# Performance work log

Measured on AMD Instinct MI355X. Metric: run time of the kernel, lower is better.

Reference implementation:

```python
import jax, jax.numpy as jnp
import numpy as np

HEADS = 24
KV_HEADS = 6
HEAD_DIM = 64


def _partial_rope(x, cos, sin):
    # x: [B, H, S, head_dim]; cos/sin: [S, rot_dim]; rotate first rot_dim dims
    rot_dim = cos.shape[-1]
    x_rot, x_pass = x[..., :rot_dim], x[..., rot_dim:]
    half = rot_dim // 2
    # use_real_unbind_dim=-2: reshape (..., 2, half) then unbind -> first/second half
    x_real, x_imag = x_rot[..., :half], x_rot[..., half:]
    x_rotated = jnp.concatenate([-x_imag, x_real], axis=-1)
    out = x_rot * cos[None, None] + x_rotated * sin[None, None]
    return jnp.concatenate([out, x_pass], axis=-1)


def setup_inputs() -> dict:
    key = jax.random.key(0)
    ks = jax.random.split(key, 8)
    B, S, D = 2, 2048, 1536
    kv_dim = KV_HEADS * HEAD_DIM
    rot_dim = 32
    hidden_states = jax.random.normal(ks[0], (B, S, D), dtype=jnp.float32)
    # realistic rotary cos/sin from inv-freq angles
    pos = jnp.arange(S, dtype=jnp.float32)
    inv_freq = 1.0 / (10000.0 ** (jnp.arange(0, rot_dim, 2, dtype=jnp.float32) / rot_dim))
    ang = pos[:, None] * inv_freq[None, :]  # [S, rot_dim//2]
    ang = jnp.concatenate([ang, ang], axis=-1)  # [S, rot_dim]
    cos, sin = jnp.cos(ang), jnp.sin(ang)
    Wq = jax.random.normal(ks[1], (D, D), dtype=jnp.float32) * 0.02
    Wk = jax.random.normal(ks[2], (D, kv_dim), dtype=jnp.float32) * 0.02
    Wv = jax.random.normal(ks[3], (D, kv_dim), dtype=jnp.float32) * 0.02
    Wo = jax.random.normal(ks[4], (D, D), dtype=jnp.float32) * 0.02
    bo = jnp.zeros((D,), dtype=jnp.float32)
    return {"hidden_states": hidden_states, "cos": cos, "sin": sin,
            "Wq": Wq, "Wk": Wk, "Wv": Wv, "Wo": Wo, "bo": bo}


def reference(hidden_states, cos, sin, Wq, Wk, Wv, Wo, bo):
    B, S, D = hidden_states.shape
    residual = hidden_states
    q = hidden_states @ Wq  # [B,S,D]
    k = hidden_states @ Wk  # [B,S,kv_dim]
    v = hidden_states @ Wv
    q = q.reshape(B, S, HEADS, HEAD_DIM).transpose(0, 2, 1, 3)       # [B,H,S,d]
    k = k.reshape(B, S, KV_HEADS, HEAD_DIM).transpose(0, 2, 1, 3)    # [B,Hkv,S,d]
    v = v.reshape(B, S, KV_HEADS, HEAD_DIM).transpose(0, 2, 1, 3)
    rep = HEADS // KV_HEADS
    k = jnp.repeat(k, rep, axis=1)  # GQA repeat_interleave -> [B,H,S,d]
    v = jnp.repeat(v, rep, axis=1)
    # partial RoPE on query and key (self-attention)
    q = _partial_rope(q, cos, sin)
    k = _partial_rope(k, cos, sin)
    scale = 1.0 / jnp.sqrt(jnp.float32(HEAD_DIM))
    scores = jnp.einsum('bhqd,bhkd->bhqk', q, k) * scale
    probs = jax.nn.softmax(scores, axis=-1)
    out = jnp.einsum('bhqk,bhkd->bhqd', probs, v)
    out = out.transpose(0, 2, 1, 3).reshape(B, S, D)
    out = out @ Wo + bo
    return out + residual
```

## Files before the change

### kernel.cpp

```cpp
#include <hip/hip_runtime.h>

#define HEADS 24
#define KVH   6
#define HD    64
#define BB    2
#define SS    2048
#define DD    1536
#define KVD   384
#define QKD   1920
#define MM    4096

typedef unsigned short ushort_t;
typedef __attribute__((ext_vector_type(8))) short short8;
typedef __attribute__((ext_vector_type(4))) short short4v;
typedef __attribute__((ext_vector_type(4))) float f32x4;

__device__ __forceinline__ ushort_t f2bf(float f) {
    union { float f; unsigned u; } v; v.f = f;
    return (ushort_t)((v.u + 0x8000u) >> 16);
}
__device__ __forceinline__ unsigned pk2(float a, float b) {
    union { float f; unsigned u; } x, y; x.f = a; y.f = b;
    return ((x.u + 0x8000u) >> 16) | (((y.u + 0x8000u) >> 16) << 16);
}
__device__ __forceinline__ unsigned pk2t(float a, float b) {
    union { float f; unsigned u; } x, y; x.f = a; y.f = b;
    return (x.u >> 16) | (y.u & 0xFFFF0000u);
}
__device__ __forceinline__ float fexp2(float s) {
    float t = fmaf(s, 8388608.0f, 1065055420.0f);
    union { int i; float f; } v; v.i = (int)t;
    return v.f;
}
__device__ __forceinline__ short8 lds_frag8(const ushort_t* p) {
    short4v lo = *(const short4v*)p;
    short4v hi = *(const short4v*)(p + 4);
    return __builtin_shufflevector(lo, hi, 0, 1, 2, 3, 4, 5, 6, 7);
}
__device__ __forceinline__ void glds16(const void* g, void* l) {
    __builtin_amdgcn_global_load_lds(
        (const __attribute__((address_space(1))) void*)g,
        (__attribute__((address_space(3))) void*)l, 16, 0, 0);
}

__device__ __forceinline__ void tconv_body(const float* __restrict__ in,
                                           ushort_t* __restrict__ out,
                                           int R, int C, int cb, int rb)
{
    __shared__ ushort_t tile[32][33];
    const int tx = threadIdx.x & 31, ty = threadIdx.x >> 5;
    const int c0 = cb * 32, r0 = rb * 32;
#pragma unroll
    for (int i = 0; i < 4; ++i)
        tile[ty + i * 8][tx] = f2bf(in[(size_t)(r0 + ty + i * 8) * C + c0 + tx]);
    __syncthreads();
#pragma unroll
    for (int i = 0; i < 4; ++i)
        out[(size_t)(c0 + ty + i * 8) * R + r0 + tx] = tile[tx][ty + i * 8];
}

#define NCVT (MM * DD / 4 / 256)
__global__ __launch_bounds__(256) void k_prep(const float* __restrict__ HS,
                                              const float* __restrict__ Wq,
                                              const float* __restrict__ Wk,
                                              const float* __restrict__ Wv,
                                              const float* __restrict__ Wo,
                                              ushort_t* __restrict__ Xbf,
                                              ushort_t* __restrict__ Wqt,
                                              ushort_t* __restrict__ Wkt,
                                              ushort_t* __restrict__ Wvt,
                                              ushort_t* __restrict__ Wot)
{
    int bid = blockIdx.x;
    if (bid < NCVT) {
        int i = bid * 256 + threadIdx.x;
        float4 v = ((const float4*)HS)[i];
        uint2 o = { pk2(v.x, v.y), pk2(v.z, v.w) };
        ((uint2*)Xbf)[i] = o;
        return;
    }
    bid -= NCVT;
    if (bid < 2304) { tconv_body(Wq, Wqt, DD, DD,  bid % 48, bid / 48); return; }
    bid -= 2304;
    if (bid < 576)  { tconv_body(Wk, Wkt, DD, KVD, bid % 12, bid / 12); return; }
    bid -= 576;
    if (bid < 576)  { tconv_body(Wv, Wvt, DD, KVD, bid % 12, bid / 12); return; }
    bid -= 576;
    tconv_body(Wo, Wot, DD, DD, bid % 48, bid / 48);
}

__global__ __launch_bounds__(256) void k_proj(const ushort_t* __restrict__ Xbf,
                                              const ushort_t* __restrict__ Wqt,
                                              const ushort_t* __restrict__ Wkt,
                                              const ushort_t* __restrict__ Wvt,
                                              const float* __restrict__ cosb,
                                              const float* __restrict__ sinb,
                                              ushort_t* __restrict__ QKVb,
                                              ushort_t* __restrict__ VT)
{
    __shared__ ushort_t As[128][32];
    __shared__ ushort_t Bs[128][32];
    const int t = threadIdx.x, lane = t & 63, wave = t >> 6;
    const int n16 = lane & 15, quad = lane >> 4;
    const int wr = wave >> 1, wc = wave & 1;
    const int srow = lane >> 2;
    const int scol = (lane & 3) * 8;

    if (blockIdx.x < 480) {
        const int nt = blockIdx.x % 15;
        const int n0 = nt * 128;
        const int m0 = (blockIdx.x / 15) * 128;
        const ushort_t* Bt; int nl, isq;
        if (nt < 12) { Bt = Wqt; nl = n0;      isq = 1; }
        else         { Bt = Wkt; nl = n0 - DD; isq = 0; }

        const size_t aoff0 = (size_t)(m0 + wave * 16 + srow) * DD + scol;
        const size_t aoff1 = (size_t)(m0 + (wave + 4) * 16 + srow) * DD + scol;
        const size_t boff0 = (size_t)(nl + wave * 16 + srow) * DD + scol;
        const size_t boff1 = (size_t)(nl + (wave + 4) * 16 + srow) * DD + scol;
        ushort_t* lA0 = &As[wave * 16][0];
        ushort_t* lA1 = &As[(wave + 4) * 16][0];
        ushort_t* lB0 = &Bs[wave * 16][0];
        ushort_t* lB1 = &Bs[(wave + 4) * 16][0];

        f32x4 acc[4][4] = {};
        for (int k0 = 0; k0 < DD; k0 += 32) {
            __syncthreads();
            glds16(Xbf + aoff0 + k0, lA0);
            glds16(Xbf + aoff1 + k0, lA1);
            glds16(Bt  + boff0 + k0, lB0);
            glds16(Bt  + boff1 + k0, lB1);
            __syncthreads();
            short8 af[4], bf8[4];
#pragma unroll
            for (int i = 0; i < 4; ++i) af[i]  = *(const short8*)&As[wr * 64 + i * 16 + n16][quad * 8];
#pragma unroll
            for (int j = 0; j < 4; ++j) bf8[j] = *(const short8*)&Bs[wc * 64 + j * 16 + n16][quad * 8];
#pragma unroll
            for (int i = 0; i < 4; ++i)
#pragma unroll
                for (int j = 0; j < 4; ++j)
                    acc[i][j] = __builtin_amdgcn_mfma_f32_16x16x32_bf16(af[i], bf8[j], acc[i][j], 0, 0, 0);
        }

        const float QSC = 0.18033688011112042f;
#pragma unroll
        for (int i = 0; i < 4; ++i) {
#pragma unroll
            for (int r = 0; r < 4; ++r) {
                const int row = m0 + wr * 64 + i * 16 + quad * 4 + r;
                ushort_t* outp = QKVb + (size_t)row * QKD + n0 + wc * 64 + n16;
                float v0 = acc[i][0][r], v1 = acc[i][1][r];
                float v2 = acc[i][2][r], v3 = acc[i][3][r];
                {
                    const int s = row & (SS - 1);
                    float c0 = cosb[s * 32 + n16],      s0 = sinb[s * 32 + n16];
                    float c1 = cosb[s * 32 + 16 + n16], s1 = sinb[s * 32 + 16 + n16];
                    float nr = v0 * c0 - v1 * s0;
                    float ni = v1 * c1 + v0 * s1;
                    v0 = nr; v1 = ni;
                }
                if (isq) { v0 *= QSC; v1 *= QSC; v2 *= QSC; v3 *= QSC; }
                outp[0]  = f2bf(v0);
                outp[16] = f2bf(v1);
                outp[32] = f2bf(v2);
                outp[48] = f2bf(v3);
            }
        }
    } else {
        const int vb = blockIdx.x - 480;
        const int n0 = (vb & 31) * 128;
        const int m0 = (vb >> 5) * 64;

        const size_t aoff  = (size_t)(m0 + wave * 16 + srow) * DD + scol;
        const size_t boff0 = (size_t)(n0 + wave * 32 + srow) * DD + scol;
        const size_t boff1 = boff0 + (size_t)16 * DD;
        ushort_t* lA  = &As[wave * 16][0];
        ushort_t* lB0 = &Bs[wave * 32][0];
        ushort_t* lB1 = &Bs[wave * 32 + 16][0];

        f32x4 acc[2][4] = {};
        for (int k0 = 0; k0 < DD; k0 += 32) {
            __syncthreads();
            glds16(Wvt + aoff  + k0, lA);
            glds16(Xbf + boff0 + k0, lB0);
            glds16(Xbf + boff1 + k0, lB1);
            __syncthreads();
            short8 af[2], bf8[4];
#pragma unroll
            for (int i = 0; i < 2; ++i) af[i]  = *(const short8*)&As[wr * 32 + i * 16 + n16][quad * 8];
#pragma unroll
            for (int j = 0; j < 4; ++j) bf8[j] = *(const short8*)&Bs[wc * 64 + j * 16 + n16][quad * 8];
#pragma unroll
            for (int i = 0; i < 2; ++i)
#pragma unroll
                for (int j = 0; j < 4; ++j)
                    acc[i][j] = __builtin_amdgcn_mfma_f32_16x16x32_bf16(af[i], bf8[j], acc[i][j], 0, 0, 0);
        }

        const int b = n0 >> 11;
        const int s0 = 8 * (n16 >> 2) + 2 * (n16 & 3);
#pragma unroll
        for (int i = 0; i < 2; ++i)
#pragma unroll
            for (int r = 0; r < 4; ++r) {
                const int c = m0 + wr * 32 + i * 16 + quad * 4 + r;
                ushort_t* op = VT + ((size_t)b * KVD + c) * SS +
                               (n0 & (SS - 1)) + wc * 64 + s0;
                *(unsigned*)op        = pk2(acc[i][0][r], acc[i][1][r]);
                *(unsigned*)(op + 32) = pk2(acc[i][2][r], acc[i][3][r]);
            }
    }
}

__global__ __launch_bounds__(256) void k_attn(const ushort_t* __restrict__ QKVb,
                                              const ushort_t* __restrict__ VT,
                                              ushort_t* __restrict__ AOb)
{
    __shared__ __align__(16) ushort_t Ks[2][64][76];
    __shared__ __align__(16) ushort_t Vs[2][64][76];

    const int t    = threadIdx.x;
    const int wave = t >> 6;
    const int quad = (t >> 4) & 3;
    const int n16  = t & 15;
    const int q0   = blockIdx.x * 128;
    const int h    = blockIdx.y;
    const int b    = blockIdx.z;
    const int kh   = h >> 2;

    const int sr = t >> 2;
    const int sc = (t & 3) * 8;
    const int vc = (t & 3) * 16;

    short8 qf[2][2];
#pragma unroll
    for (int m = 0; m < 2; ++m)
#pragma unroll
        for (int kc = 0; kc < 2; ++kc)
            qf[m][kc] = *(const short8*)(QKVb +
                (size_t)(b * SS + q0 + wave * 32 + m * 16 + n16) * QKD +
                h * HD + kc * 32 + quad * 8);

    float l_p[2] = {};
    f32x4 acc_o[2][4] = {};

    const ushort_t* Kbase = QKVb + (size_t)(b * SS) * QKD + DD + kh * HD;
    const ushort_t* Vbase = VT + ((size_t)b * KVD + kh * 64) * SS;

    uint4 kv0, kv1, vv0, vv1;

#define LOAD_TILE(K0) do {                                                  \
        const ushort_t* Kg = Kbase + (size_t)((K0) + sr) * QKD + sc;        \
        kv0 = *(const uint4*)(Kg);                                          \
        kv1 = *(const uint4*)(Kg + 32);                                     \
        const ushort_t* Vg = Vbase + (size_t)sr * SS + (K0) + vc;           \
        vv0 = *(const uint4*)(Vg);                                          \
        vv1 = *(const uint4*)(Vg + 8);                                      \
    } while (0)

#define WRITE_BUF(BI) do {                                                  \
        *(uint2*)&Ks[BI][sr][sc]      = make_uint2(kv0.x, kv0.y);           \
        *(uint2*)&Ks[BI][sr][sc + 4]  = make_uint2(kv0.z, kv0.w);           \
        *(uint2*)&Ks[BI][sr][sc + 32] = make_uint2(kv1.x, kv1.y);           \
        *(uint2*)&Ks[BI][sr][sc + 36] = make_uint2(kv1.z, kv1.w);           \
        *(uint2*)&Vs[BI][sr][vc]      = make_uint2(vv0.x, vv0.y);           \
        *(uint2*)&Vs[BI][sr][vc + 4]  = make_uint2(vv0.z, vv0.w);           \
        *(uint2*)&Vs[BI][sr][vc + 8]  = make_uint2(vv1.x, vv1.y);           \
        *(uint2*)&Vs[BI][sr][vc + 12] = make_uint2(vv1.z, vv1.w);           \
    } while (0)

    LOAD_TILE(0);
    WRITE_BUF(0);
    LOAD_TILE(64);
    __syncthreads();

    const int NT = SS / 64;
    for (int kt = 0; kt < NT; ++kt) {
        const int cur = kt & 1;
        const ushort_t (*Kc)[76] = Ks[cur];
        const ushort_t (*Vc)[76] = Vs[cur];

        f32x4 sT[2][4] = {};
#pragma unroll
        for (int kc = 0; kc < 2; ++kc) {
            short8 bf[4];
#pragma unroll
            for (int jj = 0; jj < 4; ++jj)
                bf[jj] = lds_frag8(&Kc[jj * 16 + n16][kc * 32 + quad * 8]);
#pragma unroll
            for (int m = 0; m < 2; ++m)
#pragma unroll
                for (int jj = 0; jj < 4; ++jj)
                    sT[m][jj] = __builtin_amdgcn_mfma_f32_16x16x32_bf16(
                        bf[jj], qf[m][kc], sT[m][jj], 0, 0, 0);
        }

        union PB { unsigned w[4]; short8 v; };
        PB pb[2][2];
#pragma unroll
        for (int m = 0; m < 2; ++m) {
#pragma unroll
            for (int w = 0; w < 4; ++w) {
                float p0 = fexp2(sT[m][0][w]);
                float p1 = fexp2(sT[m][1][w]);
                float p2 = fexp2(sT[m][2][w]);
                float p3 = fexp2(sT[m][3][w]);
                pb[m][0].w[w] = pk2t(p0, p1);
                pb[m][1].w[w] = pk2t(p2, p3);
                l_p[m] += (p0 + p1) + (p2 + p3);
            }
        }

#pragma unroll
        for (int kc = 0; kc < 2; ++kc) {
            short8 vb[4];
#pragma unroll
            for (int dd = 0; dd < 4; ++dd)
                vb[dd] = lds_frag8(&Vc[dd * 16 + n16][kc * 32 + quad * 8]);
#pragma unroll
            for (int m = 0; m < 2; ++m)
#pragma unroll
                for (int dd = 0; dd < 4; ++dd)
                    acc_o[m][dd] = __builtin_amdgcn_mfma_f32_16x16x32_bf16(
                        vb[dd], pb[m][kc].v, acc_o[m][dd], 0, 0, 0);
        }

        if (kt + 1 < NT) {
            WRITE_BUF(cur ^ 1);
            if (kt + 2 < NT)
                LOAD_TILE((kt + 2) * 64);
            __syncthreads();
        }
    }
#undef LOAD_TILE
#undef WRITE_BUF

#pragma unroll
    for (int m = 0; m < 2; ++m) {
        float s = l_p[m];
        s += __shfl_xor(s, 16);
        s += __shfl_xor(s, 32);
        const float inv = 1.0f / s;
        const int q = q0 + wave * 32 + m * 16 + n16;
        ushort_t* op = AOb + (size_t)(b * SS + q) * DD + h * HD + quad * 4;
#pragma unroll
        for (int dd = 0; dd < 4; ++dd) {
            uint2 o = { pk2(acc_o[m][dd][0] * inv, acc_o[m][dd][1] * inv),
                        pk2(acc_o[m][dd][2] * inv, acc_o[m][dd][3] * inv) };
            *(uint2*)(op + dd * 16) = o;
        }
    }
}

__global__ __launch_bounds__(256) void k_out_mfma(const ushort_t* __restrict__ AOb,
                                                  const ushort_t* __restrict__ Wot,
                                                  const float* __restrict__ bo,
                                                  const float* __restrict__ HS,
                                                  float* __restrict__ out)
{
    __shared__ ushort_t As[64][32];
    __shared__ ushort_t Bs[128][32];
    const int t = threadIdx.x, lane = t & 63, wave = t >> 6;
    const int n16 = lane & 15, quad = lane >> 4;
    const int wr = wave >> 1, wc = wave & 1;
    const int n0 = blockIdx.x * 128;
    const int m0 = blockIdx.y * 64;

    const int srow = lane >> 2;
    const int scol = (lane & 3) * 8;
    const size_t aoff  = (size_t)(m0 + wave * 16 + srow) * DD + scol;
    const size_t boff0 = (size_t)(n0 + wave * 32 + srow) * DD + scol;
    const size_t boff1 = boff0 + (size_t)16 * DD;
    ushort_t* lA  = &As[wave * 16][0];
    ushort_t* lB0 = &Bs[wave * 32][0];
    ushort_t* lB1 = &Bs[wave * 32 + 16][0];

    f32x4 acc[2][4] = {};
    for (int k0 = 0; k0 < DD; k0 += 32) {
        __syncthreads();
        glds16(AOb + aoff  + k0, lA);
        glds16(Wot + boff0 + k0, lB0);
        glds16(Wot + boff1 + k0, lB1);
        __syncthreads();
        short8 af[2], bf8[4];
#pragma unroll
        for (int i = 0; i < 2; ++i) af[i]  = *(const short8*)&As[wr * 32 + i * 16 + n16][quad * 8];
#pragma unroll
        for (int j = 0; j < 4; ++j) bf8[j] = *(const short8*)&Bs[wc * 64 + j * 16 + n16][quad * 8];
#pragma unroll
        for (int i = 0; i < 2; ++i)
#pragma unroll
            for (int j = 0; j < 4; ++j)
                acc[i][j] = __builtin_amdgcn_mfma_f32_16x16x32_bf16(af[i], bf8[j], acc[i][j], 0, 0, 0);
    }

    const int colb = n0 + wc * 64 + n16;
    float bo4[4];
#pragma unroll
    for (int j = 0; j < 4; ++j) bo4[j] = bo[colb + j * 16];
#pragma unroll
    for (int i = 0; i < 2; ++i) {
#pragma unroll
        for (int r = 0; r < 4; ++r) {
            const int row = m0 + wr * 32 + i * 16 + quad * 4 + r;
            float* op = out + (size_t)row * DD + colb;
            const float* hp = HS + (size_t)row * DD + colb;
#pragma unroll
            for (int j = 0; j < 4; ++j)
                op[j * 16] = acc[i][j][r] + bo4[j] + hp[j * 16];
        }
    }
}

extern "C" void kernel_launch(void* const* d_in, const int* in_sizes, int n_in,
                              void* d_out, int out_size, void* d_ws, size_t ws_size,
                              hipStream_t stream)
{
    const float* HS   = (const float*)d_in[0];
    const float* cosb = (const float*)d_in[1];
    const float* sinb = (const float*)d_in[2];
    const float* Wq   = (const float*)d_in[3];
    const float* Wk   = (const float*)d_in[4];
    const float* Wv   = (const float*)d_in[5];
    const float* Wo   = (const float*)d_in[6];
    const float* bo   = (const float*)d_in[7];
    float* out = (float*)d_out;

    ushort_t* Xbf  = (ushort_t*)d_ws;
    ushort_t* QKVb = Xbf  + (size_t)MM * DD;
    ushort_t* AOb  = QKVb + (size_t)MM * QKD;
    ushort_t* Wqt  = AOb  + (size_t)MM * DD;
    ushort_t* Wkt  = Wqt  + (size_t)DD * DD;
    ushort_t* Wvt  = Wkt  + (size_t)KVD * DD;
    ushort_t* Wot  = Wvt  + (size_t)KVD * DD;
    ushort_t* VT   = Wot  + (size_t)DD * DD;

    const int nprep = NCVT + 2304 + 576 + 576 + 2304;
    k_prep    <<<dim3(nprep), 256, 0, stream>>>(HS, Wq, Wk, Wv, Wo,
                                                Xbf, Wqt, Wkt, Wvt, Wot);
    k_proj    <<<dim3(480 + 192), 256, 0, stream>>>(Xbf, Wqt, Wkt, Wvt,
                                                    cosb, sinb, QKVb, VT);
    k_attn    <<<dim3(SS / 128, HEADS, BB), 256, 0, stream>>>(QKVb, VT, AOb);
    k_out_mfma<<<dim3(DD / 128, MM / 64),   256, 0, stream>>>(AOb, Wot, bo, HS, out);
}
```

Before: 251.6 us.

## Double-buffer LDS tiles in projection and output GEMMs to overlap loads

Gives the projection and output-projection GEMM kernels two LDS buffers per operand. The next K-slice is issued with global-to-LDS loads while MFMAs run on the current slice, and each iteration uses one barrier instead of two. The aim is to hide global load latency behind compute. LDS use per block doubles, which could reduce occupancy, and because the glds16 loads are asynchronous the single trailing barrier may not wait for them to finish unless a vmcnt wait is also emitted.

Result: slower. 269.0 us (+6.9%).

```diff
diff --git a/kernel.cpp b/kernel.cpp
--- a/kernel.cpp
+++ b/kernel.cpp
@@ -98,8 +98,8 @@
                                               ushort_t* __restrict__ QKVb,
                                               ushort_t* __restrict__ VT)
 {
-    __shared__ ushort_t As[128][32];
-    __shared__ ushort_t Bs[128][32];
+    __shared__ ushort_t As[2][128][32];
+    __shared__ ushort_t Bs[2][128][32];
     const int t = threadIdx.x, lane = t & 63, wave = t >> 6;
     const int n16 = lane & 15, quad = lane >> 4;
     const int wr = wave >> 1, wc = wave & 1;
@@ -118,29 +118,33 @@
         const size_t aoff1 = (size_t)(m0 + (wave + 4) * 16 + srow) * DD + scol;
         const size_t boff0 = (size_t)(nl + wave * 16 + srow) * DD + scol;
         const size_t boff1 = (size_t)(nl + (wave + 4) * 16 + srow) * DD + scol;
-        ushort_t* lA0 = &As[wave * 16][0];
-        ushort_t* lA1 = &As[(wave + 4) * 16][0];
-        ushort_t* lB0 = &Bs[wave * 16][0];
-        ushort_t* lB1 = &Bs[(wave + 4) * 16][0];
 
         f32x4 acc[4][4] = {};
+        glds16(Xbf + aoff0, &As[0][wave * 16][0]);
+        glds16(Xbf + aoff1, &As[0][(wave + 4) * 16][0]);
+        glds16(Bt  + boff0, &Bs[0][wave * 16][0]);
+        glds16(Bt  + boff1, &Bs[0][(wave + 4) * 16][0]);
+        __syncthreads();
         for (int k0 = 0; k0 < DD; k0 += 32) {
-            __syncthreads();
-            glds16(Xbf + aoff0 + k0, lA0);
-            glds16(Xbf + aoff1 + k0, lA1);
-            glds16(Bt  + boff0 + k0, lB0);
-            glds16(Bt  + boff1 + k0, lB1);
-            __syncthreads();
+            const int cur = (k0 >> 5) & 1;
+            if (k0 + 32 < DD) {
+                const int nk = k0 + 32;
+                glds16(Xbf + aoff0 + nk, &As[cur ^ 1][wave * 16][0]);
+                glds16(Xbf + aoff1 + nk, &As[cur ^ 1][(wave + 4) * 16][0]);
+                glds16(Bt  + boff0 + nk, &Bs[cur ^ 1][wave * 16][0]);
+                glds16(Bt  + boff1 + nk, &Bs[cur ^ 1][(wave + 4) * 16][0]);
+            }
             short8 af[4], bf8[4];
 #pragma unroll
-            for (int i = 0; i < 4; ++i) af[i]  = *(const short8*)&As[wr * 64 + i * 16 + n16][quad * 8];
-#pragma unroll
-            for (int j = 0; j < 4; ++j) bf8[j] = *(const short8*)&Bs[wc * 64 + j * 16 + n16][quad * 8];
+            for (int i = 0; i < 4; ++i) af[i]  = *(const short8*)&As[cur][wr * 64 + i * 16 + n16][quad * 8];
+#pragma unroll
+            for (int j = 0; j < 4; ++j) bf8[j] = *(const short8*)&Bs[cur][wc * 64 + j * 16 + n16][quad * 8];
 #pragma unroll
             for (int i = 0; i < 4; ++i)
 #pragma unroll
                 for (int j = 0; j < 4; ++j)
                     acc[i][j] = __builtin_amdgcn_mfma_f32_16x16x32_bf16(af[i], bf8[j], acc[i][j], 0, 0, 0);
+            __syncthreads();
         }
 
         const float QSC = 0.18033688011112042f;
@@ -175,27 +179,31 @@
         const size_t aoff  = (size_t)(m0 + wave * 16 + srow) * DD + scol;
         const size_t boff0 = (size_t)(n0 + wave * 32 + srow) * DD + scol;
         const size_t boff1 = boff0 + (size_t)16 * DD;
-        ushort_t* lA  = &As[wave * 16][0];
-        ushort_t* lB0 = &Bs[wave * 32][0];
-        ushort_t* lB1 = &Bs[wave * 32 + 16][0];
 
         f32x4 acc[2][4] = {};
+        glds16(Wvt + aoff,  &As[0][wave * 16][0]);
+        glds16(Xbf + boff0, &Bs[0][wave * 32][0]);
+        glds16(Xbf + boff1, &Bs[0][wave * 32 + 16][0]);
+        __syncthreads();
         for (int k0 = 0; k0 < DD; k0 += 32) {
-            __syncthreads();
-            glds16(Wvt + aoff  + k0, lA);
-            glds16(Xbf + boff0 + k0, lB0);
-            glds16(Xbf + boff1 + k0, lB1);
-            __syncthreads();
+            const int cur = (k0 >> 5) & 1;
+            if (k0 + 32 < DD) {
+                const int nk = k0 + 32;
+                glds16(Wvt + aoff  + nk, &As[cur ^ 1][wave * 16][0]);
+                glds16(Xbf + boff0 + nk, &Bs[cur ^ 1][wave * 32][0]);
+                glds16(Xbf + boff1 + nk, &Bs[cur ^ 1][wave * 32 + 16][0]);
+            }
             short8 af[2], bf8[4];
 #pragma unroll
-            for (int i = 0; i < 2; ++i) af[i]  = *(const short8*)&As[wr * 32 + i * 16 + n16][quad * 8];
-#pragma unroll
-            for (int j = 0; j < 4; ++j) bf8[j] = *(const short8*)&Bs[wc * 64 + j * 16 + n16][quad * 8];
+            for (int i = 0; i < 2; ++i) af[i]  = *(const short8*)&As[cur][wr * 32 + i * 16 + n16][quad * 8];
+#pragma unroll
+            for (int j = 0; j < 4; ++j) bf8[j] = *(const short8*)&Bs[cur][wc * 64 + j * 16 + n16][quad * 8];
 #pragma unroll
             for (int i = 0; i < 2; ++i)
 #pragma unroll
                 for (int j = 0; j < 4; ++j)
                     acc[i][j] = __builtin_amdgcn_mfma_f32_16x16x32_bf16(af[i], bf8[j], acc[i][j], 0, 0, 0);
+            __syncthreads();
         }
 
         const int b = n0 >> 11;
@@ -359,8 +367,8 @@
                                                   const float* __restrict__ HS,
                                                   float* __restrict__ out)
 {
-    __shared__ ushort_t As[64][32];
-    __shared__ ushort_t Bs[128][32];
+    __shared__ ushort_t As[2][64][32];
+    __shared__ ushort_t Bs[2][128][32];
     const int t = threadIdx.x, lane = t & 63, wave = t >> 6;
     const int n16 = lane & 15, quad = lane >> 4;
     const int wr = wave >> 1, wc = wave & 1;
@@ -372,27 +380,31 @@
     const size_t aoff  = (size_t)(m0 + wave * 16 + srow) * DD + scol;
     const size_t boff0 = (size_t)(n0 + wave * 32 + srow) * DD + scol;
     const size_t boff1 = boff0 + (size_t)16 * DD;
-    ushort_t* lA  = &As[wave * 16][0];
-    ushort_t* lB0 = &Bs[wave * 32][0];
-    ushort_t* lB1 = &Bs[wave * 32 + 16][0];
 
     f32x4 acc[2][4] = {};
+    glds16(AOb + aoff,  &As[0][wave * 16][0]);
+    glds16(Wot + boff0, &Bs[0][wave * 32][0]);
+    glds16(Wot + boff1, &Bs[0][wave * 32 + 16][0]);
+    __syncthreads();
     for (int k0 = 0; k0 < DD; k0 += 32) {
-        __syncthreads();
-        glds16(AOb + aoff  + k0, lA);
-        glds16(Wot + boff0 + k0, lB0);
-        glds16(Wot + boff1 + k0, lB1);
-        __syncthreads();
+        const int cur = (k0 >> 5) & 1;
+        if (k0 + 32 < DD) {
+            const int nk = k0 + 32;
+            glds16(AOb + aoff  + nk, &As[cur ^ 1][wave * 16][0]);
+            glds16(Wot + boff0 + nk, &Bs[cur ^ 1][wave * 32][0]);
+            glds16(Wot + boff1 + nk, &Bs[cur ^ 1][wave * 32 + 16][0]);
+        }
         short8 af[2], bf8[4];
 #pragma unroll
-        for (int i = 0; i < 2; ++i) af[i]  = *(const short8*)&As[wr * 32 + i * 16 + n16][quad * 8];
-#pragma unroll
-        for (int j = 0; j < 4; ++j) bf8[j] = *(const short8*)&Bs[wc * 64 + j * 16 + n16][quad * 8];
+        for (int i = 0; i < 2; ++i) af[i]  = *(const short8*)&As[cur][wr * 32 + i * 16 + n16][quad * 8];
+#pragma unroll
+        for (int j = 0; j < 4; ++j) bf8[j] = *(const short8*)&Bs[cur][wc * 64 + j * 16 + n16][quad * 8];
 #pragma unroll
         for (int i = 0; i < 2; ++i)
 #pragma unroll
             for (int j = 0; j < 4; ++j)
                 acc[i][j] = __builtin_amdgcn_mfma_f32_16x16x32_bf16(af[i], bf8[j], acc[i][j], 0, 0, 0);
+        __syncthreads();
     }
 
     const int colb = n0 + wc * 64 + n16;
```

## Split attention work across 8 waves with 16 query rows each

Applied to the files above, without the earlier changes.

The attention kernel now launches 512 threads per block, and each of the 8 waves handles 16 query rows instead of 32. This halves the per-wave accumulator and Q-fragment registers and halves the per-thread K/V tile load work, with the aim of raising occupancy and latency hiding. In exchange, each K/V LDS fragment feeds only one query tile instead of two, so LDS read traffic per MFMA doubles and more waves contend at each barrier.

Result: no change. 248.1 us (-1.4%).

```diff
diff --git a/kernel.cpp b/kernel.cpp
--- a/kernel.cpp
+++ b/kernel.cpp
@@ -213,9 +213,9 @@
     }
 }
 
-__global__ __launch_bounds__(256) void k_attn(const ushort_t* __restrict__ QKVb,
-                                              const ushort_t* __restrict__ VT,
-                                              ushort_t* __restrict__ AOb)
+__global__ __launch_bounds__(512, 6) void k_attn(const ushort_t* __restrict__ QKVb,
+                                                 const ushort_t* __restrict__ VT,
+                                                 ushort_t* __restrict__ AOb)
 {
     __shared__ __align__(16) ushort_t Ks[2][64][76];
     __shared__ __align__(16) ushort_t Vs[2][64][76];
@@ -229,45 +229,34 @@
     const int b    = blockIdx.z;
     const int kh   = h >> 2;
 
-    const int sr = t >> 2;
-    const int sc = (t & 3) * 8;
-    const int vc = (t & 3) * 16;
-
-    short8 qf[2][2];
-#pragma unroll
-    for (int m = 0; m < 2; ++m)
-#pragma unroll
-        for (int kc = 0; kc < 2; ++kc)
-            qf[m][kc] = *(const short8*)(QKVb +
-                (size_t)(b * SS + q0 + wave * 32 + m * 16 + n16) * QKD +
-                h * HD + kc * 32 + quad * 8);
-
-    float l_p[2] = {};
-    f32x4 acc_o[2][4] = {};
+    const int sr = t >> 3;
+    const int sc = (t & 7) * 8;
+
+    short8 qf[2];
+#pragma unroll
+    for (int kc = 0; kc < 2; ++kc)
+        qf[kc] = *(const short8*)(QKVb +
+            (size_t)(b * SS + q0 + wave * 16 + n16) * QKD +
+            h * HD + kc * 32 + quad * 8);
+
+    float l_p = 0.0f;
+    f32x4 acc_o[4] = {};
 
     const ushort_t* Kbase = QKVb + (size_t)(b * SS) * QKD + DD + kh * HD;
     const ushort_t* Vbase = VT + ((size_t)b * KVD + kh * 64) * SS;
 
-    uint4 kv0, kv1, vv0, vv1;
+    uint4 kv, vv;
 
 #define LOAD_TILE(K0) do {                                                  \
-        const ushort_t* Kg = Kbase + (size_t)((K0) + sr) * QKD + sc;        \
-        kv0 = *(const uint4*)(Kg);                                          \
-        kv1 = *(const uint4*)(Kg + 32);                                     \
-        const ushort_t* Vg = Vbase + (size_t)sr * SS + (K0) + vc;           \
-        vv0 = *(const uint4*)(Vg);                                          \
-        vv1 = *(const uint4*)(Vg + 8);                                      \
+        kv = *(const uint4*)(Kbase + (size_t)((K0) + sr) * QKD + sc);       \
+        vv = *(const uint4*)(Vbase + (size_t)sr * SS + (K0) + sc);          \
     } while (0)
 
 #define WRITE_BUF(BI) do {                                                  \
-        *(uint2*)&Ks[BI][sr][sc]      = make_uint2(kv0.x, kv0.y);           \
-        *(uint2*)&Ks[BI][sr][sc + 4]  = make_uint2(kv0.z, kv0.w);           \
-        *(uint2*)&Ks[BI][sr][sc + 32] = make_uint2(kv1.x, kv1.y);           \
-        *(uint2*)&Ks[BI][sr][sc + 36] = make_uint2(kv1.z, kv1.w);           \
-        *(uint2*)&Vs[BI][sr][vc]      = make_uint2(vv0.x, vv0.y);           \
-        *(uint2*)&Vs[BI][sr][vc + 4]  = make_uint2(vv0.z, vv0.w);           \
-        *(uint2*)&Vs[BI][sr][vc + 8]  = make_uint2(vv1.x, vv1.y);           \
-        *(uint2*)&Vs[BI][sr][vc + 12] = make_uint2(vv1.z, vv1.w);           \
+        *(uint2*)&Ks[BI][sr][sc]     = make_uint2(kv.x, kv.y);              \
+        *(uint2*)&Ks[BI][sr][sc + 4] = make_uint2(kv.z, kv.w);              \
+        *(uint2*)&Vs[BI][sr][sc]     = make_uint2(vv.x, vv.y);              \
+        *(uint2*)&Vs[BI][sr][sc + 4] = make_uint2(vv.z, vv.w);              \
     } while (0)
 
     LOAD_TILE(0);
@@ -281,7 +270,7 @@
         const ushort_t (*Kc)[76] = Ks[cur];
         const ushort_t (*Vc)[76] = Vs[cur];
 
-        f32x4 sT[2][4] = {};
+        f32x4 sT[4] = {};
 #pragma unroll
         for (int kc = 0; kc < 2; ++kc) {
             short8 bf[4];
@@ -289,27 +278,22 @@
             for (int jj = 0; jj < 4; ++jj)
                 bf[jj] = lds_frag8(&Kc[jj * 16 + n16][kc * 32 + quad * 8]);
 #pragma unroll
-            for (int m = 0; m < 2; ++m)
-#pragma unroll
-                for (int jj = 0; jj < 4; ++jj)
-                    sT[m][jj] = __builtin_amdgcn_mfma_f32_16x16x32_bf16(
-                        bf[jj], qf[m][kc], sT[m][jj], 0, 0, 0);
+            for (int jj = 0; jj < 4; ++jj)
+                sT[jj] = __builtin_amdgcn_mfma_f32_16x16x32_bf16(
+                    bf[jj], qf[kc], sT[jj], 0, 0, 0);
         }
 
         union PB { unsigned w[4]; short8 v; };
-        PB pb[2][2];
-#pragma unroll
-        for (int m = 0; m < 2; ++m) {
-#pragma unroll
-            for (int w = 0; w < 4; ++w) {
-                float p0 = fexp2(sT[m][0][w]);
-                float p1 = fexp2(sT[m][1][w]);
-                float p2 = fexp2(sT[m][2][w]);
-                float p3 = fexp2(sT[m][3][w]);
-                pb[m][0].w[w] = pk2t(p0, p1);
-                pb[m][1].w[w] = pk2t(p2, p3);
-                l_p[m] += (p0 + p1) + (p2 + p3);
-            }
+        PB pb[2];
+#pragma unroll
+        for (int w = 0; w < 4; ++w) {
+            float p0 = fexp2(sT[0][w]);
+            float p1 = fexp2(sT[1][w]);
+            float p2 = fexp2(sT[2][w]);
+            float p3 = fexp2(sT[3][w]);
+            pb[0].w[w] = pk2t(p0, p1);
+            pb[1].w[w] = pk2t(p2, p3);
+            l_p += (p0 + p1) + (p2 + p3);
         }
 
 #pragma unroll
@@ -319,11 +303,9 @@
             for (int dd = 0; dd < 4; ++dd)
                 vb[dd] = lds_frag8(&Vc[dd * 16 + n16][kc * 32 + quad * 8]);
 #pragma unroll
-            for (int m = 0; m < 2; ++m)
-#pragma unroll
-                for (int dd = 0; dd < 4; ++dd)
-                    acc_o[m][dd] = __builtin_amdgcn_mfma_f32_16x16x32_bf16(
-                        vb[dd], pb[m][kc].v, acc_o[m][dd], 0, 0, 0);
+            for (int dd = 0; dd < 4; ++dd)
+                acc_o[dd] = __builtin_amdgcn_mfma_f32_16x16x32_bf16(
+                    vb[dd], pb[kc].v, acc_o[dd], 0, 0, 0);
         }
 
         if (kt + 1 < NT) {
@@ -336,18 +318,17 @@
 #undef LOAD_TILE
 #undef WRITE_BUF
 
-#pragma unroll
-    for (int m = 0; m < 2; ++m) {
-        float s = l_p[m];
+    {
+        float s = l_p;
         s += __shfl_xor(s, 16);
         s += __shfl_xor(s, 32);
         const float inv = 1.0f / s;
-        const int q = q0 + wave * 32 + m * 16 + n16;
+        const int q = q0 + wave * 16 + n16;
         ushort_t* op = AOb + (size_t)(b * SS + q) * DD + h * HD + quad * 4;
 #pragma unroll
         for (int dd = 0; dd < 4; ++dd) {
-            uint2 o = { pk2(acc_o[m][dd][0] * inv, acc_o[m][dd][1] * inv),
-                        pk2(acc_o[m][dd][2] * inv, acc_o[m][dd][3] * inv) };
+            uint2 o = { pk2(acc_o[dd][0] * inv, acc_o[dd][1] * inv),
+                        pk2(acc_o[dd][2] * inv, acc_o[dd][3] * inv) };
             *(uint2*)(op + dd * 16) = o;
         }
     }
@@ -441,6 +422,6 @@
                                                 Xbf, Wqt, Wkt, Wvt, Wot);
     k_proj    <<<dim3(480 + 192), 256, 0, stream>>>(Xbf, Wqt, Wkt, Wvt,
                                                     cosb, sinb, QKVb, VT);
-    k_attn    <<<dim3(SS / 128, HEADS, BB), 256, 0, stream>>>(QKVb, VT, AOb);
+    k_attn    <<<dim3(SS / 128, HEADS, BB), 512, 0, stream>>>(QKVb, VT, AOb);
     k_out_mfma<<<dim3(DD / 128, MM / 64),   256, 0, stream>>>(AOb, Wot, bo, HS, out);
 }
```

## Split attention KV sequence across two wave groups per block with LDS reduction

Applied to the files above, without the earlier changes.

The attention kernel now launches 512 threads per block. Two groups of four waves each process alternating 64-key tiles for the same 128 queries, so the work within a block is split along the key dimension. The partial outputs and row sums are combined through an LDS scratch area at the end before normalization. This doubles the wave-level parallelism and the loads per step, but it drops the double-buffered prefetch overlap, adds an extra barrier per iteration and a final reduction, and may lower occupancy.

Measured after the change: 304.1 us. 20.9% more time.

```diff
diff --git a/kernel.cpp b/kernel.cpp
--- a/kernel.cpp
+++ b/kernel.cpp
@@ -213,25 +213,29 @@
     }
 }
 
-__global__ __launch_bounds__(256) void k_attn(const ushort_t* __restrict__ QKVb,
-                                              const ushort_t* __restrict__ VT,
-                                              ushort_t* __restrict__ AOb)
-{
-    __shared__ __align__(16) ushort_t Ks[2][64][76];
-    __shared__ __align__(16) ushort_t Vs[2][64][76];
+__global__ __launch_bounds__(512, 4) void k_attn(const ushort_t* __restrict__ QKVb,
+                                                 const ushort_t* __restrict__ VT,
+                                                 ushort_t* __restrict__ AOb)
+{
+    __shared__ __align__(16) ushort_t SMEM[2][2][64][76];
 
     const int t    = threadIdx.x;
     const int wave = t >> 6;
+    const int qg   = wave & 3;
+    const int par  = wave >> 2;
     const int quad = (t >> 4) & 3;
     const int n16  = t & 15;
+    const int lane = t & 63;
     const int q0   = blockIdx.x * 128;
     const int h    = blockIdx.y;
     const int b    = blockIdx.z;
     const int kh   = h >> 2;
 
-    const int sr = t >> 2;
-    const int sc = (t & 3) * 8;
-    const int vc = (t & 3) * 16;
+    const int ps = t >> 8;
+    const int tt = t & 255;
+    const int sr = tt >> 2;
+    const int sc = (tt & 3) * 8;
+    const int vc = (tt & 3) * 16;
 
     short8 qf[2][2];
 #pragma unroll
@@ -239,7 +243,7 @@
 #pragma unroll
         for (int kc = 0; kc < 2; ++kc)
             qf[m][kc] = *(const short8*)(QKVb +
-                (size_t)(b * SS + q0 + wave * 32 + m * 16 + n16) * QKD +
+                (size_t)(b * SS + q0 + qg * 32 + m * 16 + n16) * QKD +
                 h * HD + kc * 32 + quad * 8);
 
     float l_p[2] = {};
@@ -250,36 +254,36 @@
 
     uint4 kv0, kv1, vv0, vv1;
 
-#define LOAD_TILE(K0) do {                                                  \
-        const ushort_t* Kg = Kbase + (size_t)((K0) + sr) * QKD + sc;        \
+#define LOAD_PAIR(I) do {                                                   \
+        const int k0s = ((I) * 2 + ps) * 64;                                \
+        const ushort_t* Kg = Kbase + (size_t)(k0s + sr) * QKD + sc;         \
         kv0 = *(const uint4*)(Kg);                                          \
         kv1 = *(const uint4*)(Kg + 32);                                     \
-        const ushort_t* Vg = Vbase + (size_t)sr * SS + (K0) + vc;           \
+        const ushort_t* Vg = Vbase + (size_t)sr * SS + k0s + vc;            \
         vv0 = *(const uint4*)(Vg);                                          \
         vv1 = *(const uint4*)(Vg + 8);                                      \
     } while (0)
 
-#define WRITE_BUF(BI) do {                                                  \
-        *(uint2*)&Ks[BI][sr][sc]      = make_uint2(kv0.x, kv0.y);           \
-        *(uint2*)&Ks[BI][sr][sc + 4]  = make_uint2(kv0.z, kv0.w);           \
-        *(uint2*)&Ks[BI][sr][sc + 32] = make_uint2(kv1.x, kv1.y);           \
-        *(uint2*)&Ks[BI][sr][sc + 36] = make_uint2(kv1.z, kv1.w);           \
-        *(uint2*)&Vs[BI][sr][vc]      = make_uint2(vv0.x, vv0.y);           \
-        *(uint2*)&Vs[BI][sr][vc + 4]  = make_uint2(vv0.z, vv0.w);           \
-        *(uint2*)&Vs[BI][sr][vc + 8]  = make_uint2(vv1.x, vv1.y);           \
-        *(uint2*)&Vs[BI][sr][vc + 12] = make_uint2(vv1.z, vv1.w);           \
+#define WRITE_PAIR() do {                                                   \
+        *(uint2*)&SMEM[0][ps][sr][sc]      = make_uint2(kv0.x, kv0.y);      \
+        *(uint2*)&SMEM[0][ps][sr][sc + 4]  = make_uint2(kv0.z, kv0.w);      \
+        *(uint2*)&SMEM[0][ps][sr][sc + 32] = make_uint2(kv1.x, kv1.y);      \
+        *(uint2*)&SMEM[0][ps][sr][sc + 36] = make_uint2(kv1.z, kv1.w);      \
+        *(uint2*)&SMEM[1][ps][sr][vc]      = make_uint2(vv0.x, vv0.y);      \
+        *(uint2*)&SMEM[1][ps][sr][vc + 4]  = make_uint2(vv0.z, vv0.w);      \
+        *(uint2*)&SMEM[1][ps][sr][vc + 8]  = make_uint2(vv1.x, vv1.y);      \
+        *(uint2*)&SMEM[1][ps][sr][vc + 12] = make_uint2(vv1.z, vv1.w);      \
     } while (0)
 
-    LOAD_TILE(0);
-    WRITE_BUF(0);
-    LOAD_TILE(64);
+    LOAD_PAIR(0);
+    WRITE_PAIR();
+    LOAD_PAIR(1);
     __syncthreads();
 
-    const int NT = SS / 64;
-    for (int kt = 0; kt < NT; ++kt) {
-        const int cur = kt & 1;
-        const ushort_t (*Kc)[76] = Ks[cur];
-        const ushort_t (*Vc)[76] = Vs[cur];
+    const int NP = SS / 128;
+    for (int i = 0; i < NP; ++i) {
+        const ushort_t (*Kc)[76] = SMEM[0][par];
+        const ushort_t (*Vc)[76] = SMEM[1][par];
 
         f32x4 sT[2][4] = {};
 #pragma unroll
@@ -326,29 +330,58 @@
                         vb[dd], pb[m][kc].v, acc_o[m][dd], 0, 0, 0);
         }
 
-        if (kt + 1 < NT) {
-            WRITE_BUF(cur ^ 1);
-            if (kt + 2 < NT)
-                LOAD_TILE((kt + 2) * 64);
-            __syncthreads();
-        }
-    }
-#undef LOAD_TILE
-#undef WRITE_BUF
-
-#pragma unroll
-    for (int m = 0; m < 2; ++m) {
-        float s = l_p[m];
-        s += __shfl_xor(s, 16);
-        s += __shfl_xor(s, 32);
-        const float inv = 1.0f / s;
-        const int q = q0 + wave * 32 + m * 16 + n16;
-        ushort_t* op = AOb + (size_t)(b * SS + q) * DD + h * HD + quad * 4;
-#pragma unroll
-        for (int dd = 0; dd < 4; ++dd) {
-            uint2 o = { pk2(acc_o[m][dd][0] * inv, acc_o[m][dd][1] * inv),
-                        pk2(acc_o[m][dd][2] * inv, acc_o[m][dd][3] * inv) };
-            *(uint2*)(op + dd * 16) = o;
+        if (i + 1 < NP) {
+            __syncthreads();
+            WRITE_PAIR();
+            if (i + 2 < NP)
+                LOAD_PAIR(i + 2);
+            __syncthreads();
+        }
+    }
+#undef LOAD_PAIR
+#undef WRITE_PAIR
+
+    __syncthreads();
+    float* scr = (float*)&SMEM[0][0][0][0];
+    if (par == 1) {
+        float* p = scr + (size_t)(qg * 64 + lane) * 34;
+#pragma unroll
+        for (int m = 0; m < 2; ++m)
+#pragma unroll
+            for (int dd = 0; dd < 4; ++dd)
+#pragma unroll
+                for (int r = 0; r < 4; ++r)
+                    p[m * 16 + dd * 4 + r] = acc_o[m][dd][r];
+        p[32] = l_p[0];
+        p[33] = l_p[1];
+    }
+    __syncthreads();
+    if (par == 0) {
+        const float* p = scr + (size_t)(qg * 64 + lane) * 34;
+#pragma unroll
+        for (int m = 0; m < 2; ++m)
+#pragma unroll
+            for (int dd = 0; dd < 4; ++dd)
+#pragma unroll
+                for (int r = 0; r < 4; ++r)
+                    acc_o[m][dd][r] += p[m * 16 + dd * 4 + r];
+        l_p[0] += p[32];
+        l_p[1] += p[33];
+
+#pragma unroll
+        for (int m = 0; m < 2; ++m) {
+            float s = l_p[m];
+            s += __shfl_xor(s, 16);
+            s += __shfl_xor(s, 32);
+            const float inv = 1.0f / s;
+            const int q = q0 + qg * 32 + m * 16 + n16;
+            ushort_t* op = AOb + (size_t)(b * SS + q) * DD + h * HD + quad * 4;
+#pragma unroll
+            for (int dd = 0; dd < 4; ++dd) {
+                uint2 o = { pk2(acc_o[m][dd][0] * inv, acc_o[m][dd][1] * inv),
+                            pk2(acc_o[m][dd][2] * inv, acc_o[m][dd][3] * inv) };
+                *(uint2*)(op + dd * 16) = o;
+            }
         }
     }
 }
@@ -441,6 +474,6 @@
                                                 Xbf, Wqt, Wkt, Wvt, Wot);
     k_proj    <<<dim3(480 + 192), 256, 0, stream>>>(Xbf, Wqt, Wkt, Wvt,
                                                     cosb, sinb, QKVb, VT);
-    k_attn    <<<dim3(SS / 128, HEADS, BB), 256, 0, stream>>>(QKVb, VT, AOb);
+    k_attn    <<<dim3(SS / 128, HEADS, BB), 512, 0, stream>>>(QKVb, VT, AOb);
     k_out_mfma<<<dim3(DD / 128, MM / 64),   256, 0, stream>>>(AOb, Wot, bo, HS, out);
 }
```
